# Optimization experiments

Hardware: AMD Instinct MI355X
Metric: run time of the kernel (lower is better)

Reference implementation:

```python
import jax, jax.numpy as jnp
import numpy as np

N_NODES = 100000
N_EDGES = 1600000
F_IN = 256
F_OUT = 128


def setup_inputs() -> dict:
    key = jax.random.key(0)
    k1, k2, k3, k4, k5, k6 = jax.random.split(key, 6)
    x = jax.random.normal(k1, (N_NODES, F_IN), dtype=jnp.float32)
    edge_row = jax.random.randint(k2, (N_EDGES,), 0, N_NODES, dtype=jnp.int64 if jax.config.jax_enable_x64 else jnp.int32)
    edge_col = jax.random.randint(k3, (N_EDGES,), 0, N_NODES, dtype=jnp.int64 if jax.config.jax_enable_x64 else jnp.int32)
    edge_val = jax.random.uniform(k4, (N_EDGES,), dtype=jnp.float32)
    stdv = 1.0 / np.sqrt(F_OUT)
    weight = jax.random.uniform(k5, (F_IN, F_OUT), dtype=jnp.float32, minval=-stdv, maxval=stdv)
    bias = jax.random.uniform(k6, (F_OUT,), dtype=jnp.float32, minval=-stdv, maxval=stdv)
    return {"x": x, "edge_row": edge_row, "edge_col": edge_col,
            "edge_val": edge_val, "weight": weight, "bias": bias}


def reference(x, edge_row, edge_col, edge_val, weight, bias):
    # support = X @ W  (dense GEMM), shape [N, F_out]
    support = x @ weight
    # out = A @ support with A given in COO form: out[r] += val * support[c]
    msgs = support[edge_col] * edge_val[:, None]            # [E, F_out]
    out = jax.ops.segment_sum(msgs, edge_row, num_segments=N_NODES)
    return out + bias
```

## Files before the change

kernel.cpp:

```cpp
#include <hip/hip_runtime.h>

#define F_IN 256
#define F_OUT 128

typedef __bf16 bf16x8 __attribute__((ext_vector_type(8)));
typedef float f32x4 __attribute__((ext_vector_type(4)));

union bfbits { __bf16 b; short s; };

__global__ __launch_bounds__(256) void conv_w(const float* __restrict__ W,
                                              short* __restrict__ WTh,
                                              short* __restrict__ WTl) {
    int idx = blockIdx.x * 256 + threadIdx.x;
    if (idx >= F_IN * F_OUT) return;
    int k = idx >> 7, c = idx & 127;
    float f = W[idx];
    __bf16 h = (__bf16)f;
    float r = f - (float)h;
    __bf16 l = (__bf16)r;
    bfbits uh, ul; uh.b = h; ul.b = l;
    WTh[c * F_IN + k] = uh.s;
    WTl[c * F_IN + k] = ul.s;
}

__global__ __launch_bounds__(256, 2) void gemm_mfma(const float* __restrict__ X,
                                                    const short* __restrict__ WTh,
                                                    const short* __restrict__ WTl,
                                                    float* __restrict__ S, int M) {
    const int lane = threadIdx.x & 63;
    const int wave = threadIdx.x >> 6;
    const int lr = lane & 15;
    const int kg = lane >> 4;
    const long long rowbase = (long long)blockIdx.x * 256 + wave * 64;

    f32x4 acc[4][8];
#pragma unroll
    for (int m = 0; m < 4; m++)
#pragma unroll
        for (int n = 0; n < 8; n++) acc[m][n] = (f32x4){0.f, 0.f, 0.f, 0.f};

#pragma unroll
    for (int ks = 0; ks < 8; ks++) {
        const int k0 = ks * 32 + 8 * kg;
        bf16x8 ahi[4], alo[4];
#pragma unroll
        for (int m = 0; m < 4; m++) {
            long long r = rowbase + m * 16 + lr;
            if (r >= M) r = M - 1;
            const float* p = X + r * F_IN + k0;
            float4 f0 = *reinterpret_cast<const float4*>(p);
            float4 f1 = *reinterpret_cast<const float4*>(p + 4);
            float fv[8] = {f0.x, f0.y, f0.z, f0.w, f1.x, f1.y, f1.z, f1.w};
#pragma unroll
            for (int i = 0; i < 8; i++) {
                __bf16 h = (__bf16)fv[i];
                float res = fv[i] - (float)h;
                ahi[m][i] = h;
                alo[m][i] = (__bf16)res;
            }
        }
#pragma unroll
        for (int n = 0; n < 8; n++) {
            const int boff = (n * 16 + lr) * F_IN + k0;
            bf16x8 bhi = *reinterpret_cast<const bf16x8*>(WTh + boff);
            bf16x8 blo = *reinterpret_cast<const bf16x8*>(WTl + boff);
#pragma unroll
            for (int m = 0; m < 4; m++) {
                acc[m][n] = __builtin_amdgcn_mfma_f32_16x16x32_bf16(ahi[m], bhi, acc[m][n], 0, 0, 0);
                acc[m][n] = __builtin_amdgcn_mfma_f32_16x16x32_bf16(ahi[m], blo, acc[m][n], 0, 0, 0);
                acc[m][n] = __builtin_amdgcn_mfma_f32_16x16x32_bf16(alo[m], bhi, acc[m][n], 0, 0, 0);
            }
        }
    }
#pragma unroll
    for (int m = 0; m < 4; m++) {
#pragma unroll
        for (int j = 0; j < 4; j++) {
            long long r = rowbase + m * 16 + kg * 4 + j;
            if (r >= M) continue;
            float* orow = S + r * F_OUT + lr;
#pragma unroll
            for (int n = 0; n < 8; n++) orow[n * 16] = acc[m][n][j];
        }
    }
}

__global__ __launch_bounds__(256) void hist_rows(const int* __restrict__ erow,
                                                 int* __restrict__ cnt, int E) {
    for (int e = blockIdx.x * blockDim.x + threadIdx.x; e < E;
         e += gridDim.x * blockDim.x)
        atomicAdd(&cnt[erow[e]], 1);
}

__global__ __launch_bounds__(1024) void scan_partial(const int* __restrict__ cnt,
                                                     int* __restrict__ rp,
                                                     int* __restrict__ bsum, int N) {
    __shared__ int sm[1024];
    int t = threadIdx.x;
    int i = blockIdx.x * 1024 + t;
    int v = (i < N) ? cnt[i] : 0;
    sm[t] = v;
    __syncthreads();
#pragma unroll
    for (int off = 1; off < 1024; off <<= 1) {
        int add = (t >= off) ? sm[t - off] : 0;
        __syncthreads();
        sm[t] += add;
        __syncthreads();
    }
    if (i < N) rp[i] = sm[t] - v;
    if (t == 1023) bsum[blockIdx.x] = sm[t];
}

__global__ void scan_bsum(int* bsum, int nb) {
    __shared__ int sm[128];
    int t = threadIdx.x;
    int v = (t < nb) ? bsum[t] : 0;
    sm[t] = v;
    __syncthreads();
#pragma unroll
    for (int off = 1; off < 128; off <<= 1) {
        int add = (t >= off) ? sm[t - off] : 0;
        __syncthreads();
        sm[t] += add;
        __syncthreads();
    }
    if (t < nb) bsum[t] = sm[t] - v;
}

__global__ __launch_bounds__(256) void scan_add(int* __restrict__ rp,
                                                int* __restrict__ cursor,
                                                const int* __restrict__ bsum,
                                                int N, int E) {
    int i = blockIdx.x * 256 + threadIdx.x;
    if (i < N) {
        int v = rp[i] + bsum[i >> 10];
        rp[i] = v;
        cursor[i] = v;
    }
    if (i == 0) rp[N] = E;
}

__global__ __launch_bounds__(256) void bucket_edges(const int* __restrict__ erow,
                                                    const int* __restrict__ ecol,
                                                    const float* __restrict__ eval,
                                                    int* __restrict__ cursor,
                                                    int* __restrict__ ccol,
                                                    float* __restrict__ cval, int E) {
    int e = blockIdx.x * 256 + threadIdx.x;
    if (e >= E) return;
    int r = erow[e];
    int pos = atomicAdd(&cursor[r], 1);
    ccol[pos] = ecol[e];
    cval[pos] = eval[e];
}

__global__ __launch_bounds__(256) void gather_rows(const float* __restrict__ support,
                                                   const int* __restrict__ rp,
                                                   const int* __restrict__ ccol,
                                                   const float* __restrict__ cval,
                                                   const float* __restrict__ bias,
                                                   float* __restrict__ out, int N) {
    int wid = (blockIdx.x * 256 + threadIdx.x) >> 6;
    int lane = threadIdx.x & 63;
    if (wid >= N) return;
    int s = rp[wid], e = rp[wid + 1];
    const float2* S2 = reinterpret_cast<const float2*>(support);
    float2 acc = reinterpret_cast<const float2*>(bias)[lane];
    int i = s;
    for (; i + 4 <= e; i += 4) {
        int c0 = ccol[i], c1 = ccol[i + 1], c2 = ccol[i + 2], c3 = ccol[i + 3];
        float v0 = cval[i], v1 = cval[i + 1], v2 = cval[i + 2], v3 = cval[i + 3];
        float2 s0 = S2[(size_t)c0 * 64 + lane];
        float2 s1 = S2[(size_t)c1 * 64 + lane];
        float2 s2 = S2[(size_t)c2 * 64 + lane];
        float2 s3 = S2[(size_t)c3 * 64 + lane];
        acc.x = fmaf(v0, s0.x, acc.x); acc.y = fmaf(v0, s0.y, acc.y);
        acc.x = fmaf(v1, s1.x, acc.x); acc.y = fmaf(v1, s1.y, acc.y);
        acc.x = fmaf(v2, s2.x, acc.x); acc.y = fmaf(v2, s2.y, acc.y);
        acc.x = fmaf(v3, s3.x, acc.x); acc.y = fmaf(v3, s3.y, acc.y);
    }
    for (; i < e; i++) {
        int c = ccol[i];
        float v = cval[i];
        float2 sv = S2[(size_t)c * 64 + lane];
        acc.x = fmaf(v, sv.x, acc.x);
        acc.y = fmaf(v, sv.y, acc.y);
    }
    reinterpret_cast<float2*>(out)[(size_t)wid * 64 + lane] = acc;
}

extern "C" void kernel_launch(void* const* d_in, const int* in_sizes, int n_in,
                              void* d_out, int out_size, void* d_ws, size_t ws_size,
                              hipStream_t stream) {
    const float* x    = (const float*)d_in[0];
    const int*   erow = (const int*)d_in[1];
    const int*   ecol = (const int*)d_in[2];
    const float* eval = (const float*)d_in[3];
    const float* w    = (const float*)d_in[4];
    const float* bias = (const float*)d_in[5];
    float* out = (float*)d_out;

    const int M = in_sizes[0] / F_IN;
    const int E = in_sizes[1];

    char* ws = (char*)d_ws;
    float* support = (float*)(ws);
    int*   ccol    = (int*)  (ws + 51200000);
    float* cval    = (float*)(ws + 57600000);
    int*   rp      = (int*)  (ws + 64000000);
    int*   cursor  = (int*)  (ws + 64400064);
    int*   bsum    = (int*)  (ws + 64800064);
    short* WTh     = (short*)(ws + 51200000);
    short* WTl     = (short*)(ws + 51265536);

    conv_w<<<(F_IN * F_OUT + 255) / 256, 256, 0, stream>>>(w, WTh, WTl);

    gemm_mfma<<<(M + 255) / 256, 256, 0, stream>>>(x, WTh, WTl, support, M);

    hipMemsetAsync(cursor, 0, (size_t)M * 4, stream);
    hist_rows<<<2048, 256, 0, stream>>>(erow, cursor, E);
    int nb = (M + 1023) / 1024;
    scan_partial<<<nb, 1024, 0, stream>>>(cursor, rp, bsum, M);
    scan_bsum<<<1, 128, 0, stream>>>(bsum, nb);
    scan_add<<<(M + 255) / 256, 256, 0, stream>>>(rp, cursor, bsum, M, E);
    bucket_edges<<<(E + 255) / 256, 256, 0, stream>>>(erow, ecol, eval, cursor, ccol, cval, E);

    gather_rows<<<((size_t)M * 64 + 255) / 256, 256, 0, stream>>>(support, rp, ccol, cval, bias, out, M);
}
```

Baseline: 495.9 us.

## Record atomic rank in histogram and build edge permutation instead of bucketed copies

The histogram pass now stores each edge's atomic return value as a per-row rank. The bucketing pass then writes only a permutation index at rp[row]+rank, with no second atomic, and no longer copies col/val. The gather kernel reads col and val indirectly through the permutation and unrolls the edge loop by 8 to keep more loads in flight. This removes the second atomic pass and two scattered writes, at the cost of an extra indirection and uncoalesced reads of ecol/eval in the gather.

```diff
diff --git a/kernel.cpp b/kernel.cpp
--- a/kernel.cpp
+++ b/kernel.cpp
@@ -85,11 +85,12 @@
     }
 }
 
-__global__ __launch_bounds__(256) void hist_rows(const int* __restrict__ erow,
-                                                 int* __restrict__ cnt, int E) {
+__global__ __launch_bounds__(256) void hist_rank(const int* __restrict__ erow,
+                                                 int* __restrict__ cnt,
+                                                 int* __restrict__ rank, int E) {
     for (int e = blockIdx.x * blockDim.x + threadIdx.x; e < E;
          e += gridDim.x * blockDim.x)
-        atomicAdd(&cnt[erow[e]], 1);
+        rank[e] = atomicAdd(&cnt[erow[e]], 1);
 }
 
 __global__ __launch_bounds__(1024) void scan_partial(const int* __restrict__ cnt,
@@ -129,36 +130,27 @@
 }
 
 __global__ __launch_bounds__(256) void scan_add(int* __restrict__ rp,
-                                                int* __restrict__ cursor,
                                                 const int* __restrict__ bsum,
                                                 int N, int E) {
     int i = blockIdx.x * 256 + threadIdx.x;
-    if (i < N) {
-        int v = rp[i] + bsum[i >> 10];
-        rp[i] = v;
-        cursor[i] = v;
-    }
+    if (i < N) rp[i] += bsum[i >> 10];
     if (i == 0) rp[N] = E;
 }
 
-__global__ __launch_bounds__(256) void bucket_edges(const int* __restrict__ erow,
-                                                    const int* __restrict__ ecol,
-                                                    const float* __restrict__ eval,
-                                                    int* __restrict__ cursor,
-                                                    int* __restrict__ ccol,
-                                                    float* __restrict__ cval, int E) {
+__global__ __launch_bounds__(256) void bucket_perm(const int* __restrict__ erow,
+                                                   const int* __restrict__ rank,
+                                                   const int* __restrict__ rp,
+                                                   int* __restrict__ perm, int E) {
     int e = blockIdx.x * 256 + threadIdx.x;
     if (e >= E) return;
-    int r = erow[e];
-    int pos = atomicAdd(&cursor[r], 1);
-    ccol[pos] = ecol[e];
-    cval[pos] = eval[e];
+    perm[rp[erow[e]] + rank[e]] = e;
 }
 
 __global__ __launch_bounds__(256) void gather_rows(const float* __restrict__ support,
                                                    const int* __restrict__ rp,
-                                                   const int* __restrict__ ccol,
-                                                   const float* __restrict__ cval,
+                                                   const int* __restrict__ perm,
+                                                   const int* __restrict__ ecol,
+                                                   const float* __restrict__ eval,
                                                    const float* __restrict__ bias,
                                                    float* __restrict__ out, int N) {
     int wid = (blockIdx.x * 256 + threadIdx.x) >> 6;
@@ -168,21 +160,38 @@
     const float2* S2 = reinterpret_cast<const float2*>(support);
     float2 acc = reinterpret_cast<const float2*>(bias)[lane];
     int i = s;
+    for (; i + 8 <= e; i += 8) {
+        int ee[8]; int cc[8]; float vv[8]; float2 ss[8];
+#pragma unroll
+        for (int j = 0; j < 8; j++) ee[j] = perm[i + j];
+#pragma unroll
+        for (int j = 0; j < 8; j++) { cc[j] = ecol[ee[j]]; vv[j] = eval[ee[j]]; }
+#pragma unroll
+        for (int j = 0; j < 8; j++) ss[j] = S2[(size_t)cc[j] * 64 + lane];
+#pragma unroll
+        for (int j = 0; j < 8; j++) {
+            acc.x = fmaf(vv[j], ss[j].x, acc.x);
+            acc.y = fmaf(vv[j], ss[j].y, acc.y);
+        }
+    }
     for (; i + 4 <= e; i += 4) {
-        int c0 = ccol[i], c1 = ccol[i + 1], c2 = ccol[i + 2], c3 = ccol[i + 3];
-        float v0 = cval[i], v1 = cval[i + 1], v2 = cval[i + 2], v3 = cval[i + 3];
-        float2 s0 = S2[(size_t)c0 * 64 + lane];
-        float2 s1 = S2[(size_t)c1 * 64 + lane];
-        float2 s2 = S2[(size_t)c2 * 64 + lane];
-        float2 s3 = S2[(size_t)c3 * 64 + lane];
-        acc.x = fmaf(v0, s0.x, acc.x); acc.y = fmaf(v0, s0.y, acc.y);
-        acc.x = fmaf(v1, s1.x, acc.x); acc.y = fmaf(v1, s1.y, acc.y);
-        acc.x = fmaf(v2, s2.x, acc.x); acc.y = fmaf(v2, s2.y, acc.y);
-        acc.x = fmaf(v3, s3.x, acc.x); acc.y = fmaf(v3, s3.y, acc.y);
+        int ee[4]; int cc[4]; float vv[4]; float2 ss[4];
+#pragma unroll
+        for (int j = 0; j < 4; j++) ee[j] = perm[i + j];
+#pragma unroll
+        for (int j = 0; j < 4; j++) { cc[j] = ecol[ee[j]]; vv[j] = eval[ee[j]]; }
+#pragma unroll
+        for (int j = 0; j < 4; j++) ss[j] = S2[(size_t)cc[j] * 64 + lane];
+#pragma unroll
+        for (int j = 0; j < 4; j++) {
+            acc.x = fmaf(vv[j], ss[j].x, acc.x);
+            acc.y = fmaf(vv[j], ss[j].y, acc.y);
+        }
     }
     for (; i < e; i++) {
-        int c = ccol[i];
-        float v = cval[i];
+        int e0 = perm[i];
+        int c = ecol[e0];
+        float v = eval[e0];
         float2 sv = S2[(size_t)c * 64 + lane];
         acc.x = fmaf(v, sv.x, acc.x);
         acc.y = fmaf(v, sv.y, acc.y);
@@ -206,10 +215,10 @@
 
     char* ws = (char*)d_ws;
     float* support = (float*)(ws);
-    int*   ccol    = (int*)  (ws + 51200000);
-    float* cval    = (float*)(ws + 57600000);
+    int*   perm    = (int*)  (ws + 51200000);
+    int*   rank    = (int*)  (ws + 57600000);
     int*   rp      = (int*)  (ws + 64000000);
-    int*   cursor  = (int*)  (ws + 64400064);
+    int*   cnt     = (int*)  (ws + 64400064);
     int*   bsum    = (int*)  (ws + 64800064);
     short* WTh     = (short*)(ws + 51200000);
     short* WTl     = (short*)(ws + 51265536);
@@ -218,13 +227,13 @@
 
     gemm_mfma<<<(M + 255) / 256, 256, 0, stream>>>(x, WTh, WTl, support, M);
 
-    hipMemsetAsync(cursor, 0, (size_t)M * 4, stream);
-    hist_rows<<<2048, 256, 0, stream>>>(erow, cursor, E);
+    hipMemsetAsync(cnt, 0, (size_t)M * 4, stream);
+    hist_rank<<<2048, 256, 0, stream>>>(erow, cnt, rank, E);
     int nb = (M + 1023) / 1024;
-    scan_partial<<<nb, 1024, 0, stream>>>(cursor, rp, bsum, M);
+    scan_partial<<<nb, 1024, 0, stream>>>(cnt, rp, bsum, M);
     scan_bsum<<<1, 128, 0, stream>>>(bsum, nb);
-    scan_add<<<(M + 255) / 256, 256, 0, stream>>>(rp, cursor, bsum, M, E);
-    bucket_edges<<<(E + 255) / 256, 256, 0, stream>>>(erow, ecol, eval, cursor, ccol, cval, E);
-
-    gather_rows<<<((size_t)M * 64 + 255) / 256, 256, 0, stream>>>(support, rp, ccol, cval, bias, out, M);
-}
+    scan_add<<<(M + 255) / 256, 256, 0, stream>>>(rp, bsum, M, E);
+    bucket_perm<<<(E + 255) / 256, 256, 0, stream>>>(erow, rank, rp, perm, E);
+
+    gather_rows<<<((size_t)M * 64 + 255) / 256, 256, 0, stream>>>(support, rp, perm, ecol, eval, bias, out, M);
+}
```

New measurement: 466.8 us. -5.9%, faster.
